# Kernel optimization log

Measured on AMD Instinct MI355X. Metric: run time of the kernel, lower is better.

The kernel has to match this reference:

```python
import jax, jax.numpy as jnp
import numpy as np

N = 50000
E = 600000
F_IN = 128
F_OUT = 128


def setup_inputs() -> dict:
    key = jax.random.key(0)
    k = jax.random.split(key, 8)
    x = jax.random.normal(k[0], (N, F_IN), dtype=jnp.float32)
    edge_index = jax.random.randint(k[1], (2, E), 0, N, dtype=jnp.int64)
    edge_weight = jax.random.uniform(k[2], (E,), dtype=jnp.float32)
    # glorot-initialized linear params (w1 is dead code in the original, kept for faithfulness)
    s = float(np.sqrt(6.0 / (F_IN + F_OUT)))
    W1 = jax.random.uniform(k[3], (F_IN, F_OUT), minval=-s, maxval=s, dtype=jnp.float32)
    b1 = jnp.zeros((F_OUT,), dtype=jnp.float32)
    W2 = jax.random.uniform(k[4], (F_IN, F_OUT), minval=-s, maxval=s, dtype=jnp.float32)
    b2 = jnp.zeros((F_OUT,), dtype=jnp.float32)
    a = jnp.full((1,), 0.5, dtype=jnp.float32)
    b = jnp.full((1,), 0.5, dtype=jnp.float32)
    return {"x": x, "edge_index": edge_index, "edge_weight": edge_weight,
            "W1": W1, "b1": b1, "W2": W2, "b2": b2, "a": a, "b": b}


def reference(x, edge_index, edge_weight, W1, b1, W2, b2, a, b):
    # wh_1 = self.w1(x)  (computed but unused in the original forward)
    wh_1 = x @ W1 + b1  # noqa: F841 (dead, DCE'd under jit)
    src, dst = edge_index[0], edge_index[1]
    # gather neighbor features [E, F_IN], scatter-sum to destination nodes [N, F_IN]
    x_j = jax.ops.segment_sum(x[src], dst, num_segments=N)
    wh_2 = x_j @ W2 + b2
    return wh_2
```

## Files before the change

kernel.cpp:

```cpp
#include <hip/hip_runtime.h>

#define F 128
#define CAP 64
#define LDT 136
#define TR 64
#define KC 32
#define LDA 36
#define LDW 160

typedef __attribute__((ext_vector_type(8))) short bf16x8;
typedef __attribute__((ext_vector_type(4))) float f32x4;

__device__ __forceinline__ unsigned short bf16r(float f)
{
    unsigned u = __float_as_uint(f);
    return (unsigned short)((u + 0x7fffu + ((u >> 16) & 1u)) >> 16);
}

__device__ __forceinline__ void load_edge(const int* __restrict__ ei, int is64,
                                          int E, int e, int& s, int& d)
{
    if (is64) {
        s = reinterpret_cast<const int2*>(ei)[e].x;
        d = reinterpret_cast<const int2*>(ei)[(size_t)E + e].x;
    } else {
        s = ei[e];
        d = ei[E + e];
    }
}

__global__ __launch_bounds__(256) void prep_kernel(
    const int* __restrict__ ei, const float* __restrict__ x,
    const float* __restrict__ W, int* __restrict__ flag,
    int* __restrict__ cursor, unsigned int* __restrict__ xh,
    unsigned short* __restrict__ Wt, int N, int M)
{
    int i = blockIdx.x * 256 + threadIdx.x;
    if (i < M) {
        float2 v = reinterpret_cast<const float2*>(x)[i];
        xh[i] = (unsigned)bf16r(v.x) | ((unsigned)bf16r(v.y) << 16);
    }
    if (i < N) cursor[i] = 0;
    if (i < F * F) {
        int k = i >> 7, n = i & 127;
        Wt[n * F + k] = bf16r(W[i]);
    }
    if (i == 0) {
        int or_hi = ei[1] | ei[3] | ei[5] | ei[7] | ei[9] | ei[11] | ei[13] | ei[15];
        *flag = (or_hi == 0) ? 1 : 0;
    }
}

__global__ __launch_bounds__(256) void position4_kernel(
    const int* __restrict__ ei, const int* __restrict__ flag_p,
    int* __restrict__ cursor, unsigned short* __restrict__ csr16, int E)
{
    const int tid = blockIdx.x * 256 + threadIdx.x;
    const int base = 4 * tid;
    if (base >= E) return;
    const int is64 = *flag_p;

    int s[4], d[4];
    int cnt;
    if (base + 3 < E && (E & 3) == 0) {
        cnt = 4;
        if (is64) {
            const int4* sp = reinterpret_cast<const int4*>(ei);
            int4 a = sp[tid * 2], b = sp[tid * 2 + 1];
            s[0] = a.x; s[1] = a.z; s[2] = b.x; s[3] = b.z;
            const int4* dp = reinterpret_cast<const int4*>(ei) + ((size_t)E >> 1);
            int4 c = dp[tid * 2], e4 = dp[tid * 2 + 1];
            d[0] = c.x; d[1] = c.z; d[2] = e4.x; d[3] = e4.z;
        } else {
            int4 sv = reinterpret_cast<const int4*>(ei)[tid];
            int4 dv = reinterpret_cast<const int4*>(ei + E)[tid];
            s[0] = sv.x; s[1] = sv.y; s[2] = sv.z; s[3] = sv.w;
            d[0] = dv.x; d[1] = dv.y; d[2] = dv.z; d[3] = dv.w;
        }
    } else {
        cnt = E - base; if (cnt > 4) cnt = 4;
        for (int j = 0; j < cnt; ++j) load_edge(ei, is64, E, base + j, s[j], d[j]);
        for (int j = cnt; j < 4; ++j) { s[j] = 0; d[j] = 0; }
    }

    int slot[4];
    #pragma unroll
    for (int j = 0; j < 4; ++j)
        slot[j] = (j < cnt) ? atomicAdd(&cursor[d[j]], 1) : CAP;
    #pragma unroll
    for (int j = 0; j < 4; ++j)
        if (slot[j] < CAP) csr16[(size_t)d[j] * CAP + slot[j]] = (unsigned short)s[j];
}

__device__ __forceinline__ float4 bf16x4_to_f4(uint2 u)
{
    float4 f;
    f.x = __uint_as_float(u.x << 16);
    f.y = __uint_as_float(u.x & 0xffff0000u);
    f.z = __uint_as_float(u.y << 16);
    f.w = __uint_as_float(u.y & 0xffff0000u);
    return f;
}

__global__ __launch_bounds__(256) void gather_bucket_kernel(
    const unsigned int* __restrict__ xh, const int* __restrict__ ei,
    const int* __restrict__ flag_p, const int* __restrict__ cursor,
    const unsigned short* __restrict__ csr16, unsigned int* __restrict__ aggbf,
    int N, int E)
{
    int node = blockIdx.x * 4 + (threadIdx.x >> 6);
    if (node >= N) return;
    int lane = threadIdx.x & 63;
    int half = lane >> 5;
    int col = lane & 31;
    int deg = cursor[node];

    const uint2* x2 = reinterpret_cast<const uint2*>(xh);
    float4 a0 = make_float4(0.f, 0.f, 0.f, 0.f);
    float4 a1 = make_float4(0.f, 0.f, 0.f, 0.f);

    if (deg <= CAP) {
        int sv = (lane < deg) ? (int)csr16[(size_t)node * CAP + lane] : 0;
        int i = 0;
        for (; i + 3 < deg; i += 4) {
            int e0 = __shfl(sv, i + half);
            int e1 = __shfl(sv, i + 2 + half);
            float4 v0 = bf16x4_to_f4(x2[(size_t)e0 * 32 + col]);
            float4 v1 = bf16x4_to_f4(x2[(size_t)e1 * 32 + col]);
            a0.x += v0.x; a0.y += v0.y; a0.z += v0.z; a0.w += v0.w;
            a1.x += v1.x; a1.y += v1.y; a1.z += v1.z; a1.w += v1.w;
        }
        for (; i + 1 < deg; i += 2) {
            int e0 = __shfl(sv, i + half);
            float4 v0 = bf16x4_to_f4(x2[(size_t)e0 * 32 + col]);
            a0.x += v0.x; a0.y += v0.y; a0.z += v0.z; a0.w += v0.w;
        }
        if (i < deg) {
            int e0 = __shfl(sv, i);
            if (half == 0) {
                float4 v = bf16x4_to_f4(x2[(size_t)e0 * 32 + col]);
                a0.x += v.x; a0.y += v.y; a0.z += v.z; a0.w += v.w;
            }
        }
    } else {
        int is64 = *flag_p;
        for (int base = 0; base < E; base += 64) {
            int e = base + lane;
            int s = 0, d = -1;
            if (e < E) load_edge(ei, is64, E, e, s, d);
            unsigned long long m = __ballot(d == node);
            while (m) {
                int i = __ffsll((long long)m) - 1;
                m &= m - 1;
                int sb = __shfl(s, i);
                float4 v = bf16x4_to_f4(x2[(size_t)sb * 32 + col]);
                if (half == 0) { a0.x += v.x; a0.y += v.y; a0.z += v.z; a0.w += v.w; }
            }
        }
    }
    a0.x += a1.x; a0.y += a1.y; a0.z += a1.z; a0.w += a1.w;
    a0.x += __shfl_xor(a0.x, 32);
    a0.y += __shfl_xor(a0.y, 32);
    a0.z += __shfl_xor(a0.z, 32);
    a0.w += __shfl_xor(a0.w, 32);
    if (half == 0) {
        uint2 o;
        o.x = (unsigned)bf16r(a0.x) | ((unsigned)bf16r(a0.y) << 16);
        o.y = (unsigned)bf16r(a0.z) | ((unsigned)bf16r(a0.w) << 16);
        reinterpret_cast<uint2*>(aggbf)[(size_t)node * 32 + col] = o;
    }
}

__global__ __launch_bounds__(256) void gemm_mfma_kernel(
    const unsigned short* __restrict__ aggbf, const unsigned short* __restrict__ Wt,
    const float* __restrict__ bias, float* __restrict__ out, int N)
{
    __shared__ unsigned short sWt[F * LDT];
    const int t = threadIdx.x;

    const uint4* Wg = reinterpret_cast<const uint4*>(Wt);
    #pragma unroll
    for (int u = 0; u < 8; ++u) {
        int idx = u * 256 + t;
        int n = idx >> 4;
        int c = idx & 15;
        *reinterpret_cast<uint4*>(&sWt[n * LDT + c * 8]) = Wg[idx];
    }
    __syncthreads();

    const int wv = t >> 6, lane = t & 63;
    const int quad = lane >> 4, n15 = lane & 15;
    const int rbase = blockIdx.x * 64 + wv * 16;

    f32x4 acc[8];
    #pragma unroll
    for (int i = 0; i < 8; ++i) acc[i] = (f32x4){0.f, 0.f, 0.f, 0.f};

    const int arow = rbase + n15;
    const bool aval = (arow < N);
    #pragma unroll
    for (int kc = 0; kc < F; kc += 32) {
        bf16x8 af;
        if (aval)
            af = *reinterpret_cast<const bf16x8*>(aggbf + (size_t)arow * F + kc + quad * 8);
        else
            af = (bf16x8){0, 0, 0, 0, 0, 0, 0, 0};
        #pragma unroll
        for (int nt = 0; nt < 8; ++nt) {
            bf16x8 bfr = *reinterpret_cast<const bf16x8*>(
                &sWt[(nt * 16 + n15) * LDT + kc + quad * 8]);
            acc[nt] = __builtin_amdgcn_mfma_f32_16x16x32_bf16(af, bfr, acc[nt], 0, 0, 0);
        }
    }

    #pragma unroll
    for (int nt = 0; nt < 8; ++nt) {
        float bv = bias[nt * 16 + n15];
        #pragma unroll
        for (int reg = 0; reg < 4; ++reg) {
            int row = rbase + quad * 4 + reg;
            if (row < N)
                out[(size_t)row * F + nt * 16 + n15] = acc[nt][reg] + bv;
        }
    }
}

__global__ __launch_bounds__(256) void init_kernel(
    const int* __restrict__ ei, int* __restrict__ flag,
    int* __restrict__ zero_arr, int N)
{
    int i = blockIdx.x * 256 + threadIdx.x;
    if (i < N) zero_arr[i] = 0;
    if (i == 0) {
        int or_hi = ei[1] | ei[3] | ei[5] | ei[7] | ei[9] | ei[11] | ei[13] | ei[15];
        *flag = (or_hi == 0) ? 1 : 0;
    }
}

__global__ __launch_bounds__(256) void position_bucket_kernel(
    const int* __restrict__ ei, const int* __restrict__ flag_p,
    int* __restrict__ cursor, int* __restrict__ csr_src, int E)
{
    int e = blockIdx.x * 256 + threadIdx.x;
    if (e >= E) return;
    int s, d;
    load_edge(ei, *flag_p, E, e, s, d);
    int slot = atomicAdd(&cursor[d], 1);
    if (slot < CAP) csr_src[(size_t)d * CAP + slot] = s;
}

__global__ __launch_bounds__(256) void gather_bucket_f32_kernel(
    const float* __restrict__ x, const int* __restrict__ ei,
    const int* __restrict__ flag_p, const int* __restrict__ cursor,
    const int* __restrict__ csr_src, float* __restrict__ agg, int N, int E)
{
    int node = blockIdx.x * 4 + (threadIdx.x >> 6);
    if (node >= N) return;
    int lane = threadIdx.x & 63;
    int half = lane >> 5;
    int col = lane & 31;
    int deg = cursor[node];

    const float4* x4 = reinterpret_cast<const float4*>(x);
    float4 a0 = make_float4(0.f, 0.f, 0.f, 0.f);
    float4 a1 = make_float4(0.f, 0.f, 0.f, 0.f);

    if (deg <= CAP) {
        int sv = (lane < deg) ? csr_src[(size_t)node * CAP + lane] : 0;
        int i = 0;
        for (; i + 3 < deg; i += 4) {
            int e0 = __shfl(sv, i + half);
            int e1 = __shfl(sv, i + 2 + half);
            float4 v0 = x4[(size_t)e0 * 32 + col];
            float4 v1 = x4[(size_t)e1 * 32 + col];
            a0.x += v0.x; a0.y += v0.y; a0.z += v0.z; a0.w += v0.w;
            a1.x += v1.x; a1.y += v1.y; a1.z += v1.z; a1.w += v1.w;
        }
        for (; i + 1 < deg; i += 2) {
            int e0 = __shfl(sv, i + half);
            float4 v0 = x4[(size_t)e0 * 32 + col];
            a0.x += v0.x; a0.y += v0.y; a0.z += v0.z; a0.w += v0.w;
        }
        if (i < deg) {
            int e0 = __shfl(sv, i);
            if (half == 0) {
                float4 v = x4[(size_t)e0 * 32 + col];
                a0.x += v.x; a0.y += v.y; a0.z += v.z; a0.w += v.w;
            }
        }
    } else {
        int is64 = *flag_p;
        for (int base = 0; base < E; base += 64) {
            int e = base + lane;
            int s = 0, d = -1;
            if (e < E) load_edge(ei, is64, E, e, s, d);
            unsigned long long m = __ballot(d == node);
            while (m) {
                int i = __ffsll((long long)m) - 1;
                m &= m - 1;
                int sb = __shfl(s, i);
                float4 v = x4[(size_t)sb * 32 + col];
                if (half == 0) { a0.x += v.x; a0.y += v.y; a0.z += v.z; a0.w += v.w; }
            }
        }
    }
    a0.x += a1.x; a0.y += a1.y; a0.z += a1.z; a0.w += a1.w;
    a0.x += __shfl_xor(a0.x, 32);
    a0.y += __shfl_xor(a0.y, 32);
    a0.z += __shfl_xor(a0.z, 32);
    a0.w += __shfl_xor(a0.w, 32);
    if (half == 0)
        reinterpret_cast<float4*>(agg)[(size_t)node * 32 + col] = a0;
}

__global__ __launch_bounds__(256) void scatter_kernel(
    const float* __restrict__ x, const int* __restrict__ ei,
    const int* __restrict__ flag_p, float* __restrict__ agg, int E)
{
    int tid = blockIdx.x * 256 + threadIdx.x;
    int e = tid >> 5;
    if (e >= E) return;
    int c = (tid & 31) << 2;
    int s, d;
    load_edge(ei, *flag_p, E, e, s, d);
    float4 v = *reinterpret_cast<const float4*>(x + (size_t)s * F + c);
    float* o = agg + (size_t)d * F + c;
    unsafeAtomicAdd(o + 0, v.x);
    unsafeAtomicAdd(o + 1, v.y);
    unsafeAtomicAdd(o + 2, v.z);
    unsafeAtomicAdd(o + 3, v.w);
}

__global__ __launch_bounds__(256) void gemm_kernel(
    float* __restrict__ io, const float* __restrict__ W,
    const float* __restrict__ bias, int N)
{
    __shared__ float sA[TR * LDA];
    __shared__ float sW[KC * LDW];
    const int t = threadIdx.x;
    const int row0 = blockIdx.x * TR;
    const int g = t & 7;
    const int r = t >> 3;

    float acc[2][16];
    #pragma unroll
    for (int i = 0; i < 2; ++i)
        #pragma unroll
        for (int j = 0; j < 16; ++j) acc[i][j] = 0.0f;

    for (int kc = 0; kc < F; kc += KC) {
        #pragma unroll
        for (int u = 0; u < 2; ++u) {
            int idx = u * 256 + t;
            int row = idx >> 3;
            int k4 = (idx & 7) * 4;
            int grow = row0 + row;
            float4 v = (grow < N)
                ? *reinterpret_cast<const float4*>(io + (size_t)grow * F + kc + k4)
                : make_float4(0.f, 0.f, 0.f, 0.f);
            *reinterpret_cast<float4*>(&sA[row * LDA + k4]) = v;
        }
        #pragma unroll
        for (int u = 0; u < 4; ++u) {
            int idx = u * 256 + t;
            int kk = idx >> 5;
            int f4 = (idx & 31) * 4;
            float4 v = *reinterpret_cast<const float4*>(W + (size_t)(kc + kk) * F + f4);
            int chunk = f4 >> 4;
            int within = f4 & 15;
            *reinterpret_cast<float4*>(&sW[kk * LDW + chunk * 20 + within]) = v;
        }
        __syncthreads();

        #pragma unroll 8
        for (int kk = 0; kk < KC; ++kk) {
            const float* wp = &sW[kk * LDW + g * 20];
            const float4 w0 = *reinterpret_cast<const float4*>(wp + 0);
            const float4 w1 = *reinterpret_cast<const float4*>(wp + 4);
            const float4 w2 = *reinterpret_cast<const float4*>(wp + 8);
            const float4 w3 = *reinterpret_cast<const float4*>(wp + 12);
            #pragma unroll
            for (int i = 0; i < 2; ++i) {
                const float xv = sA[(r * 2 + i) * LDA + kk];
                acc[i][0]  += xv * w0.x;  acc[i][1]  += xv * w0.y;
                acc[i][2]  += xv * w0.z;  acc[i][3]  += xv * w0.w;
                acc[i][4]  += xv * w1.x;  acc[i][5]  += xv * w1.y;
                acc[i][6]  += xv * w1.z;  acc[i][7]  += xv * w1.w;
                acc[i][8]  += xv * w2.x;  acc[i][9]  += xv * w2.y;
                acc[i][10] += xv * w2.z;  acc[i][11] += xv * w2.w;
                acc[i][12] += xv * w3.x;  acc[i][13] += xv * w3.y;
                acc[i][14] += xv * w3.z;  acc[i][15] += xv * w3.w;
            }
        }
        __syncthreads();
    }

    float bv[16];
    #pragma unroll
    for (int j = 0; j < 16; ++j) bv[j] = bias[g * 16 + j];
    #pragma unroll
    for (int i = 0; i < 2; ++i) {
        int row = row0 + r * 2 + i;
        if (row < N) {
            float* o = io + (size_t)row * F + g * 16;
            #pragma unroll
            for (int j4 = 0; j4 < 4; ++j4) {
                float4 v;
                v.x = acc[i][j4 * 4 + 0] + bv[j4 * 4 + 0];
                v.y = acc[i][j4 * 4 + 1] + bv[j4 * 4 + 1];
                v.z = acc[i][j4 * 4 + 2] + bv[j4 * 4 + 2];
                v.w = acc[i][j4 * 4 + 3] + bv[j4 * 4 + 3];
                *reinterpret_cast<float4*>(o + j4 * 4) = v;
            }
        }
    }
}

extern "C" void kernel_launch(void* const* d_in, const int* in_sizes, int n_in,
                              void* d_out, int out_size, void* d_ws, size_t ws_size,
                              hipStream_t stream) {
    const float* x  = (const float*)d_in[0];
    const int*   ei = (const int*)d_in[1];
    const float* W2 = (const float*)d_in[5];
    const float* b2 = (const float*)d_in[6];
    float* out = (float*)d_out;

    const int N = in_sizes[0] / F;
    const int E = in_sizes[2];
    const int nblk = (N + 255) / 256;
    const int M = N * (F / 2);
    const int eblk = (E + 255) / 256;

    int* ws = (int*)d_ws;
    size_t needA = (size_t)16 * 4 + (size_t)N * 4 + (size_t)N * CAP * 2
                 + (size_t)M * 4 + (size_t)F * F * 2 + (size_t)N * (F / 2) * 4;
    size_t needB = (size_t)(16 + N + (size_t)N * CAP) * sizeof(int);

    if (ws_size >= needA && N <= 65536) {
        int* flag    = ws;
        int* cursor  = flag + 16;
        unsigned short* csr16 = (unsigned short*)(cursor + N);
        unsigned int*   xh    = (unsigned int*)(csr16 + (size_t)N * CAP);
        unsigned short* Wt    = (unsigned short*)(xh + M);
        unsigned int*   aggbf = (unsigned int*)(Wt + F * F);

        int pmax = M; if (N > pmax) pmax = N; if (F * F > pmax) pmax = F * F;
        prep_kernel<<<(pmax + 255) / 256, 256, 0, stream>>>(
            ei, x, W2, flag, cursor, xh, Wt, N, M);
        int pblk = ((E + 3) / 4 + 255) / 256;
        position4_kernel<<<pblk, 256, 0, stream>>>(ei, flag, cursor, csr16, E);
        gather_bucket_kernel<<<(N + 3) / 4, 256, 0, stream>>>(
            xh, ei, flag, cursor, csr16, aggbf, N, E);
        gemm_mfma_kernel<<<(N + 63) / 64, 256, 0, stream>>>(
            (const unsigned short*)aggbf, Wt, b2, out, N);
    } else if (ws_size >= needB) {
        int* flag    = ws;
        int* cursor  = flag + 16;
        int* csr_src = cursor + N;
        init_kernel<<<nblk, 256, 0, stream>>>(ei, flag, cursor, N);
        position_bucket_kernel<<<eblk, 256, 0, stream>>>(ei, flag, cursor, csr_src, E);
        gather_bucket_f32_kernel<<<(N + 3) / 4, 256, 0, stream>>>(
            x, ei, flag, cursor, csr_src, out, N, E);
        gemm_kernel<<<(N + TR - 1) / TR, 256, 0, stream>>>(out, W2, b2, N);
    } else {
        int* flag = ws;
        init_kernel<<<1, 64, 0, stream>>>(ei, flag, flag + 16, 0);
        hipMemsetAsync(out, 0, (size_t)N * F * sizeof(float), stream);
        scatter_kernel<<<(E * 32 + 255) / 256, 256, 0, stream>>>(x, ei, flag, out, E);
        gemm_kernel<<<(N + TR - 1) / TR, 256, 0, stream>>>(out, W2, b2, N);
    }
}
```

Before: 161.5 us.

## Fuse gather into MFMA GEMM via shared memory and merge prep with CSR build

Each GEMM block now builds its 64 aggregated rows itself: every wave walks 16 nodes with a prefetched next-node CSR list and writes bf16 sums into LDS, so the aggbf round trip through global memory and one launch go away. The x/W conversion and the edge bucketing are merged into one kernel, which computes the int64 flag inline, and the cursor array is zeroed with a memset. The price is less parallelism in the gather (one wave serially handles 16 nodes, about 782 blocks), a larger LDS footprint that may limit occupancy, and a new race: the bf16 copy of x is written in the same kernel that fills the CSR, but it is only read by the next kernel, so that part is safe.

```diff
diff --git a/kernel.cpp b/kernel.cpp
--- a/kernel.cpp
+++ b/kernel.cpp
@@ -17,6 +17,11 @@
     return (unsigned short)((u + 0x7fffu + ((u >> 16) & 1u)) >> 16);
 }
 
+__device__ __forceinline__ unsigned pack2(float a, float b)
+{
+    return (unsigned)bf16r(a) | ((unsigned)bf16r(b) << 16);
+}
+
 __device__ __forceinline__ void load_edge(const int* __restrict__ ei, int is64,
                                           int E, int e, int& s, int& d)
 {
@@ -29,36 +34,40 @@
     }
 }
 
-__global__ __launch_bounds__(256) void prep_kernel(
+__device__ __forceinline__ float4 bf16x4_to_f4(uint2 u)
+{
+    float4 f;
+    f.x = __uint_as_float(u.x << 16);
+    f.y = __uint_as_float(u.x & 0xffff0000u);
+    f.z = __uint_as_float(u.y << 16);
+    f.w = __uint_as_float(u.y & 0xffff0000u);
+    return f;
+}
+
+__global__ __launch_bounds__(256) void prep_pos_kernel(
     const int* __restrict__ ei, const float* __restrict__ x,
-    const float* __restrict__ W, int* __restrict__ flag,
-    int* __restrict__ cursor, unsigned int* __restrict__ xh,
-    unsigned short* __restrict__ Wt, int N, int M)
-{
-    int i = blockIdx.x * 256 + threadIdx.x;
-    if (i < M) {
-        float2 v = reinterpret_cast<const float2*>(x)[i];
-        xh[i] = (unsigned)bf16r(v.x) | ((unsigned)bf16r(v.y) << 16);
-    }
-    if (i < N) cursor[i] = 0;
-    if (i < F * F) {
-        int k = i >> 7, n = i & 127;
-        Wt[n * F + k] = bf16r(W[i]);
-    }
-    if (i == 0) {
-        int or_hi = ei[1] | ei[3] | ei[5] | ei[7] | ei[9] | ei[11] | ei[13] | ei[15];
-        *flag = (or_hi == 0) ? 1 : 0;
-    }
-}
-
-__global__ __launch_bounds__(256) void position4_kernel(
-    const int* __restrict__ ei, const int* __restrict__ flag_p,
-    int* __restrict__ cursor, unsigned short* __restrict__ csr16, int E)
+    const float* __restrict__ W, int* __restrict__ cursor,
+    unsigned short* __restrict__ csr16, unsigned int* __restrict__ xh,
+    unsigned short* __restrict__ Wt, int N, int E, int M4)
 {
     const int tid = blockIdx.x * 256 + threadIdx.x;
+
+    if (tid < M4) {
+        float4 v = reinterpret_cast<const float4*>(x)[tid];
+        uint2 o;
+        o.x = pack2(v.x, v.y);
+        o.y = pack2(v.z, v.w);
+        reinterpret_cast<uint2*>(xh)[tid] = o;
+    }
+    if (tid < F * F) {
+        int k = tid >> 7, n = tid & 127;
+        Wt[n * F + k] = bf16r(W[tid]);
+    }
+
     const int base = 4 * tid;
     if (base >= E) return;
-    const int is64 = *flag_p;
+    int or_hi = ei[1] | ei[3] | ei[5] | ei[7] | ei[9] | ei[11] | ei[13] | ei[15];
+    const int is64 = (or_hi == 0) ? 1 : 0;
 
     int s[4], d[4];
     int cnt;
@@ -92,90 +101,14 @@
         if (slot[j] < CAP) csr16[(size_t)d[j] * CAP + slot[j]] = (unsigned short)s[j];
 }
 
-__device__ __forceinline__ float4 bf16x4_to_f4(uint2 u)
-{
-    float4 f;
-    f.x = __uint_as_float(u.x << 16);
-    f.y = __uint_as_float(u.x & 0xffff0000u);
-    f.z = __uint_as_float(u.y << 16);
-    f.w = __uint_as_float(u.y & 0xffff0000u);
-    return f;
-}
-
-__global__ __launch_bounds__(256) void gather_bucket_kernel(
+__global__ __launch_bounds__(256) void gather_gemm_kernel(
     const unsigned int* __restrict__ xh, const int* __restrict__ ei,
-    const int* __restrict__ flag_p, const int* __restrict__ cursor,
-    const unsigned short* __restrict__ csr16, unsigned int* __restrict__ aggbf,
-    int N, int E)
-{
-    int node = blockIdx.x * 4 + (threadIdx.x >> 6);
-    if (node >= N) return;
-    int lane = threadIdx.x & 63;
-    int half = lane >> 5;
-    int col = lane & 31;
-    int deg = cursor[node];
-
-    const uint2* x2 = reinterpret_cast<const uint2*>(xh);
-    float4 a0 = make_float4(0.f, 0.f, 0.f, 0.f);
-    float4 a1 = make_float4(0.f, 0.f, 0.f, 0.f);
-
-    if (deg <= CAP) {
-        int sv = (lane < deg) ? (int)csr16[(size_t)node * CAP + lane] : 0;
-        int i = 0;
-        for (; i + 3 < deg; i += 4) {
-            int e0 = __shfl(sv, i + half);
-            int e1 = __shfl(sv, i + 2 + half);
-            float4 v0 = bf16x4_to_f4(x2[(size_t)e0 * 32 + col]);
-            float4 v1 = bf16x4_to_f4(x2[(size_t)e1 * 32 + col]);
-            a0.x += v0.x; a0.y += v0.y; a0.z += v0.z; a0.w += v0.w;
-            a1.x += v1.x; a1.y += v1.y; a1.z += v1.z; a1.w += v1.w;
-        }
-        for (; i + 1 < deg; i += 2) {
-            int e0 = __shfl(sv, i + half);
-            float4 v0 = bf16x4_to_f4(x2[(size_t)e0 * 32 + col]);
-            a0.x += v0.x; a0.y += v0.y; a0.z += v0.z; a0.w += v0.w;
-        }
-        if (i < deg) {
-            int e0 = __shfl(sv, i);
-            if (half == 0) {
-                float4 v = bf16x4_to_f4(x2[(size_t)e0 * 32 + col]);
-                a0.x += v.x; a0.y += v.y; a0.z += v.z; a0.w += v.w;
-            }
-        }
-    } else {
-        int is64 = *flag_p;
-        for (int base = 0; base < E; base += 64) {
-            int e = base + lane;
-            int s = 0, d = -1;
-            if (e < E) load_edge(ei, is64, E, e, s, d);
-            unsigned long long m = __ballot(d == node);
-            while (m) {
-                int i = __ffsll((long long)m) - 1;
-                m &= m - 1;
-                int sb = __shfl(s, i);
-                float4 v = bf16x4_to_f4(x2[(size_t)sb * 32 + col]);
-                if (half == 0) { a0.x += v.x; a0.y += v.y; a0.z += v.z; a0.w += v.w; }
-            }
-        }
-    }
-    a0.x += a1.x; a0.y += a1.y; a0.z += a1.z; a0.w += a1.w;
-    a0.x += __shfl_xor(a0.x, 32);
-    a0.y += __shfl_xor(a0.y, 32);
-    a0.z += __shfl_xor(a0.z, 32);
-    a0.w += __shfl_xor(a0.w, 32);
-    if (half == 0) {
-        uint2 o;
-        o.x = (unsigned)bf16r(a0.x) | ((unsigned)bf16r(a0.y) << 16);
-        o.y = (unsigned)bf16r(a0.z) | ((unsigned)bf16r(a0.w) << 16);
-        reinterpret_cast<uint2*>(aggbf)[(size_t)node * 32 + col] = o;
-    }
-}
-
-__global__ __launch_bounds__(256) void gemm_mfma_kernel(
-    const unsigned short* __restrict__ aggbf, const unsigned short* __restrict__ Wt,
-    const float* __restrict__ bias, float* __restrict__ out, int N)
+    const int* __restrict__ cursor, const unsigned short* __restrict__ csr16,
+    const unsigned short* __restrict__ Wt, const float* __restrict__ bias,
+    float* __restrict__ out, int N, int E)
 {
     __shared__ unsigned short sWt[F * LDT];
+    __shared__ unsigned short sA[64 * LDT];
     const int t = threadIdx.x;
 
     const uint4* Wg = reinterpret_cast<const uint4*>(Wt);
@@ -186,25 +119,113 @@
         int c = idx & 15;
         *reinterpret_cast<uint4*>(&sWt[n * LDT + c * 8]) = Wg[idx];
     }
+
+    const int wv = t >> 6, lane = t & 63;
+    const int half = lane >> 5, col = lane & 31;
+    const int nbase = blockIdx.x * 64 + wv * 16;
+    const uint2* x2 = reinterpret_cast<const uint2*>(xh);
+
+    int degl = 0;
+    {
+        int myn = nbase + (lane & 15);
+        if (lane < 16 && myn < N) degl = cursor[myn];
+    }
+
+    int node = nbase;
+    int deg = __shfl(degl, 0);
+    int sv = 0;
+    if (node < N && deg <= CAP && lane < deg)
+        sv = (int)csr16[(size_t)node * CAP + lane];
+
+    for (int ni = 0; ni < 16; ++ni) {
+        int nnode = node + 1;
+        int ndeg = (ni < 15) ? __shfl(degl, ni + 1) : 0;
+        int nsv = 0;
+        if (ni < 15 && nnode < N && ndeg <= CAP && lane < ndeg)
+            nsv = (int)csr16[(size_t)nnode * CAP + lane];
+
+        float4 a0 = make_float4(0.f, 0.f, 0.f, 0.f);
+        float4 a1 = make_float4(0.f, 0.f, 0.f, 0.f);
+        if (node < N) {
+            if (deg <= CAP) {
+                int i = 0;
+                for (; i + 7 < deg; i += 8) {
+                    int e0 = __shfl(sv, i + half);
+                    int e1 = __shfl(sv, i + 2 + half);
+                    int e2 = __shfl(sv, i + 4 + half);
+                    int e3 = __shfl(sv, i + 6 + half);
+                    float4 v0 = bf16x4_to_f4(x2[(size_t)e0 * 32 + col]);
+                    float4 v1 = bf16x4_to_f4(x2[(size_t)e1 * 32 + col]);
+                    float4 v2 = bf16x4_to_f4(x2[(size_t)e2 * 32 + col]);
+                    float4 v3 = bf16x4_to_f4(x2[(size_t)e3 * 32 + col]);
+                    a0.x += v0.x; a0.y += v0.y; a0.z += v0.z; a0.w += v0.w;
+                    a1.x += v1.x; a1.y += v1.y; a1.z += v1.z; a1.w += v1.w;
+                    a0.x += v2.x; a0.y += v2.y; a0.z += v2.z; a0.w += v2.w;
+                    a1.x += v3.x; a1.y += v3.y; a1.z += v3.z; a1.w += v3.w;
+                }
+                for (; i + 3 < deg; i += 4) {
+                    int e0 = __shfl(sv, i + half);
+                    int e1 = __shfl(sv, i + 2 + half);
+                    float4 v0 = bf16x4_to_f4(x2[(size_t)e0 * 32 + col]);
+                    float4 v1 = bf16x4_to_f4(x2[(size_t)e1 * 32 + col]);
+                    a0.x += v0.x; a0.y += v0.y; a0.z += v0.z; a0.w += v0.w;
+                    a1.x += v1.x; a1.y += v1.y; a1.z += v1.z; a1.w += v1.w;
+                }
+                for (; i + 1 < deg; i += 2) {
+                    int e0 = __shfl(sv, i + half);
+                    float4 v0 = bf16x4_to_f4(x2[(size_t)e0 * 32 + col]);
+                    a0.x += v0.x; a0.y += v0.y; a0.z += v0.z; a0.w += v0.w;
+                }
+                if (i < deg) {
+                    int e0 = __shfl(sv, i);
+                    if (half == 0) {
+                        float4 v = bf16x4_to_f4(x2[(size_t)e0 * 32 + col]);
+                        a0.x += v.x; a0.y += v.y; a0.z += v.z; a0.w += v.w;
+                    }
+                }
+            } else {
+                int or_hi = ei[1] | ei[3] | ei[5] | ei[7] | ei[9] | ei[11] | ei[13] | ei[15];
+                int is64 = (or_hi == 0) ? 1 : 0;
+                for (int base = 0; base < E; base += 64) {
+                    int e = base + lane;
+                    int ss = 0, dd = -1;
+                    if (e < E) load_edge(ei, is64, E, e, ss, dd);
+                    unsigned long long m = __ballot(dd == node);
+                    while (m) {
+                        int i = __ffsll((long long)m) - 1;
+                        m &= m - 1;
+                        int sb = __shfl(ss, i);
+                        float4 v = bf16x4_to_f4(x2[(size_t)sb * 32 + col]);
+                        if (half == 0) { a0.x += v.x; a0.y += v.y; a0.z += v.z; a0.w += v.w; }
+                    }
+                }
+            }
+        }
+        a0.x += a1.x; a0.y += a1.y; a0.z += a1.z; a0.w += a1.w;
+        a0.x += __shfl_xor(a0.x, 32);
+        a0.y += __shfl_xor(a0.y, 32);
+        a0.z += __shfl_xor(a0.z, 32);
+        a0.w += __shfl_xor(a0.w, 32);
+        if (half == 0) {
+            uint2 o;
+            o.x = pack2(a0.x, a0.y);
+            o.y = pack2(a0.z, a0.w);
+            *reinterpret_cast<uint2*>(&sA[(wv * 16 + ni) * LDT + col * 4]) = o;
+        }
+        node = nnode; deg = ndeg; sv = nsv;
+    }
+
     __syncthreads();
 
-    const int wv = t >> 6, lane = t & 63;
     const int quad = lane >> 4, n15 = lane & 15;
-    const int rbase = blockIdx.x * 64 + wv * 16;
-
     f32x4 acc[8];
     #pragma unroll
     for (int i = 0; i < 8; ++i) acc[i] = (f32x4){0.f, 0.f, 0.f, 0.f};
 
-    const int arow = rbase + n15;
-    const bool aval = (arow < N);
     #pragma unroll
     for (int kc = 0; kc < F; kc += 32) {
-        bf16x8 af;
-        if (aval)
-            af = *reinterpret_cast<const bf16x8*>(aggbf + (size_t)arow * F + kc + quad * 8);
-        else
-            af = (bf16x8){0, 0, 0, 0, 0, 0, 0, 0};
+        bf16x8 af = *reinterpret_cast<const bf16x8*>(
+            &sA[(wv * 16 + n15) * LDT + kc + quad * 8]);
         #pragma unroll
         for (int nt = 0; nt < 8; ++nt) {
             bf16x8 bfr = *reinterpret_cast<const bf16x8*>(
@@ -213,6 +234,7 @@
         }
     }
 
+    const int rbase = blockIdx.x * 64 + wv * 16;
     #pragma unroll
     for (int nt = 0; nt < 8; ++nt) {
         float bv = bias[nt * 16 + n15];
@@ -416,6 +438,8 @@
     }
 }
 
+static inline size_t al16(size_t v) { return (v + 15) & ~(size_t)15; }
+
 extern "C" void kernel_launch(void* const* d_in, const int* in_sizes, int n_in,
                               void* d_out, int out_size, void* d_ws, size_t ws_size,
                               hipStream_t stream) {
@@ -428,42 +452,45 @@
     const int N = in_sizes[0] / F;
     const int E = in_sizes[2];
     const int nblk = (N + 255) / 256;
-    const int M = N * (F / 2);
     const int eblk = (E + 255) / 256;
 
-    int* ws = (int*)d_ws;
-    size_t needA = (size_t)16 * 4 + (size_t)N * 4 + (size_t)N * CAP * 2
-                 + (size_t)M * 4 + (size_t)F * F * 2 + (size_t)N * (F / 2) * 4;
+    char* wsb = (char*)d_ws;
+    size_t off = 64;
+    int* cursor = (int*)(wsb + off);
+    off = al16(off + (size_t)N * 4);
+    unsigned short* csr16 = (unsigned short*)(wsb + off);
+    off = al16(off + (size_t)N * CAP * 2);
+    unsigned int* xh = (unsigned int*)(wsb + off);
+    off = al16(off + (size_t)N * (F / 2) * 4);
+    unsigned short* Wt = (unsigned short*)(wsb + off);
+    off += (size_t)F * F * 2;
+    size_t needA = off;
+
     size_t needB = (size_t)(16 + N + (size_t)N * CAP) * sizeof(int);
 
     if (ws_size >= needA && N <= 65536) {
-        int* flag    = ws;
-        int* cursor  = flag + 16;
-        unsigned short* csr16 = (unsigned short*)(cursor + N);
-        unsigned int*   xh    = (unsigned int*)(csr16 + (size_t)N * CAP);
-        unsigned short* Wt    = (unsigned short*)(xh + M);
-        unsigned int*   aggbf = (unsigned int*)(Wt + F * F);
-
-        int pmax = M; if (N > pmax) pmax = N; if (F * F > pmax) pmax = F * F;
-        prep_kernel<<<(pmax + 255) / 256, 256, 0, stream>>>(
-            ei, x, W2, flag, cursor, xh, Wt, N, M);
-        int pblk = ((E + 3) / 4 + 255) / 256;
-        position4_kernel<<<pblk, 256, 0, stream>>>(ei, flag, cursor, csr16, E);
-        gather_bucket_kernel<<<(N + 3) / 4, 256, 0, stream>>>(
-            xh, ei, flag, cursor, csr16, aggbf, N, E);
-        gemm_mfma_kernel<<<(N + 63) / 64, 256, 0, stream>>>(
-            (const unsigned short*)aggbf, Wt, b2, out, N);
+        hipMemsetAsync(cursor, 0, (size_t)N * sizeof(int), stream);
+
+        const int M4 = N * (F / 4);
+        int gp = (M4 + 255) / 256;
+        int ge = (((E + 3) / 4) + 255) / 256; if (ge > gp) gp = ge;
+        int gw = (F * F + 255) / 256;         if (gw > gp) gp = gw;
+        prep_pos_kernel<<<gp, 256, 0, stream>>>(
+            ei, x, W2, cursor, csr16, xh, Wt, N, E, M4);
+
+        gather_gemm_kernel<<<(N + 63) / 64, 256, 0, stream>>>(
+            xh, ei, cursor, csr16, Wt, b2, out, N, E);
     } else if (ws_size >= needB) {
-        int* flag    = ws;
-        int* cursor  = flag + 16;
-        int* csr_src = cursor + N;
-        init_kernel<<<nblk, 256, 0, stream>>>(ei, flag, cursor, N);
-        position_bucket_kernel<<<eblk, 256, 0, stream>>>(ei, flag, cursor, csr_src, E);
+        int* flag    = (int*)wsb;
+        int* curs    = flag + 16;
+        int* csr_src = curs + N;
+        init_kernel<<<nblk, 256, 0, stream>>>(ei, flag, curs, N);
+        position_bucket_kernel<<<eblk, 256, 0, stream>>>(ei, flag, curs, csr_src, E);
         gather_bucket_f32_kernel<<<(N + 3) / 4, 256, 0, stream>>>(
-            x, ei, flag, cursor, csr_src, out, N, E);
+            x, ei, flag, curs, csr_src, out, N, E);
         gemm_kernel<<<(N + TR - 1) / TR, 256, 0, stream>>>(out, W2, b2, N);
     } else {
-        int* flag = ws;
+        int* flag = (int*)wsb;
         init_kernel<<<1, 64, 0, stream>>>(ei, flag, flag + 16, 0);
         hipMemsetAsync(out, 0, (size_t)N * F * sizeof(float), stream);
         scatter_kernel<<<(E * 32 + 255) / 256, 256, 0, stream>>>(x, ei, flag, out, E);
```

Measured after the change: 194.4 us. 1.2x slower.

## Gather neighbor rows via async global-to-LDS copies and widen prep conversion

Applied to the files above, without the earlier changes.

Replaces the register-based neighbor gather with global_load_lds async 16-byte copies that stage up to 16 neighbor rows per wave in LDS, then accumulate 8 bf16 values per lane with a cross-lane reduction. The aim is more bytes per load instruction and more loads in flight, hiding gather latency. The prep kernel also converts x to bf16 four floats per thread instead of two. The change adds LDS use, explicit waitcnt barriers that serialize each chunk, and wasted lanes when degree is not a multiple of 4.

```diff
diff --git a/kernel.cpp b/kernel.cpp
--- a/kernel.cpp
+++ b/kernel.cpp
@@ -17,6 +17,11 @@
     return (unsigned short)((u + 0x7fffu + ((u >> 16) & 1u)) >> 16);
 }
 
+__device__ __forceinline__ unsigned pack2(float a, float b)
+{
+    return (unsigned)bf16r(a) | ((unsigned)bf16r(b) << 16);
+}
+
 __device__ __forceinline__ void load_edge(const int* __restrict__ ei, int is64,
                                           int E, int e, int& s, int& d)
 {
@@ -29,16 +34,37 @@
     }
 }
 
+__device__ __forceinline__ float4 bf16x4_to_f4(uint2 u)
+{
+    float4 f;
+    f.x = __uint_as_float(u.x << 16);
+    f.y = __uint_as_float(u.x & 0xffff0000u);
+    f.z = __uint_as_float(u.y << 16);
+    f.w = __uint_as_float(u.y & 0xffff0000u);
+    return f;
+}
+
+__device__ __forceinline__ void async_copy16(const void* g, void* lds)
+{
+    __builtin_amdgcn_global_load_lds(
+        (const __attribute__((address_space(1))) unsigned int*)g,
+        (__attribute__((address_space(3))) unsigned int*)lds,
+        16, 0, 0);
+}
+
 __global__ __launch_bounds__(256) void prep_kernel(
     const int* __restrict__ ei, const float* __restrict__ x,
     const float* __restrict__ W, int* __restrict__ flag,
     int* __restrict__ cursor, unsigned int* __restrict__ xh,
-    unsigned short* __restrict__ Wt, int N, int M)
+    unsigned short* __restrict__ Wt, int N, int M4)
 {
     int i = blockIdx.x * 256 + threadIdx.x;
-    if (i < M) {
-        float2 v = reinterpret_cast<const float2*>(x)[i];
-        xh[i] = (unsigned)bf16r(v.x) | ((unsigned)bf16r(v.y) << 16);
+    if (i < M4) {
+        float4 v = reinterpret_cast<const float4*>(x)[i];
+        uint2 o;
+        o.x = pack2(v.x, v.y);
+        o.y = pack2(v.z, v.w);
+        reinterpret_cast<uint2*>(xh)[i] = o;
     }
     if (i < N) cursor[i] = 0;
     if (i < F * F) {
@@ -92,58 +118,77 @@
         if (slot[j] < CAP) csr16[(size_t)d[j] * CAP + slot[j]] = (unsigned short)s[j];
 }
 
-__device__ __forceinline__ float4 bf16x4_to_f4(uint2 u)
-{
-    float4 f;
-    f.x = __uint_as_float(u.x << 16);
-    f.y = __uint_as_float(u.x & 0xffff0000u);
-    f.z = __uint_as_float(u.y << 16);
-    f.w = __uint_as_float(u.y & 0xffff0000u);
-    return f;
-}
-
-__global__ __launch_bounds__(256) void gather_bucket_kernel(
+__global__ __launch_bounds__(256, 8) void gather_async_kernel(
     const unsigned int* __restrict__ xh, const int* __restrict__ ei,
     const int* __restrict__ flag_p, const int* __restrict__ cursor,
     const unsigned short* __restrict__ csr16, unsigned int* __restrict__ aggbf,
     int N, int E)
 {
-    int node = blockIdx.x * 4 + (threadIdx.x >> 6);
+    __shared__ char stg[4][4096];
+    const int node = blockIdx.x * 4 + (threadIdx.x >> 6);
     if (node >= N) return;
-    int lane = threadIdx.x & 63;
-    int half = lane >> 5;
-    int col = lane & 31;
-    int deg = cursor[node];
-
-    const uint2* x2 = reinterpret_cast<const uint2*>(xh);
-    float4 a0 = make_float4(0.f, 0.f, 0.f, 0.f);
-    float4 a1 = make_float4(0.f, 0.f, 0.f, 0.f);
+    const int wv   = threadIdx.x >> 6;
+    const int lane = threadIdx.x & 63;
+    const int eg   = lane >> 4;
+    const int c    = lane & 15;
+    char* ldsW = &stg[wv][0];
+
+    const int deg = cursor[node];
 
     if (deg <= CAP) {
         int sv = (lane < deg) ? (int)csr16[(size_t)node * CAP + lane] : 0;
-        int i = 0;
-        for (; i + 3 < deg; i += 4) {
-            int e0 = __shfl(sv, i + half);
-            int e1 = __shfl(sv, i + 2 + half);
-            float4 v0 = bf16x4_to_f4(x2[(size_t)e0 * 32 + col]);
-            float4 v1 = bf16x4_to_f4(x2[(size_t)e1 * 32 + col]);
-            a0.x += v0.x; a0.y += v0.y; a0.z += v0.z; a0.w += v0.w;
-            a1.x += v1.x; a1.y += v1.y; a1.z += v1.z; a1.w += v1.w;
-        }
-        for (; i + 1 < deg; i += 2) {
-            int e0 = __shfl(sv, i + half);
-            float4 v0 = bf16x4_to_f4(x2[(size_t)e0 * 32 + col]);
-            a0.x += v0.x; a0.y += v0.y; a0.z += v0.z; a0.w += v0.w;
-        }
-        if (i < deg) {
-            int e0 = __shfl(sv, i);
-            if (half == 0) {
-                float4 v = bf16x4_to_f4(x2[(size_t)e0 * 32 + col]);
-                a0.x += v.x; a0.y += v.y; a0.z += v.z; a0.w += v.w;
-            }
+        float f[8];
+        #pragma unroll
+        for (int j = 0; j < 8; ++j) f[j] = 0.f;
+
+        for (int ch = 0; ch < deg; ch += 16) {
+            int nE = deg - ch; if (nE > 16) nE = 16;
+            int nL = (nE + 3) >> 2;
+            if (ch > 0) {
+                asm volatile("s_waitcnt lgkmcnt(0)" ::: "memory");
+                __builtin_amdgcn_sched_barrier(0);
+            }
+            for (int l = 0; l < nL; ++l) {
+                int e = ch + l * 4 + eg;
+                int esel = (e < deg) ? e : (deg - 1);
+                int src = __shfl(sv, esel);
+                async_copy16((const char*)xh + ((size_t)src * 256 + (size_t)c * 16),
+                             ldsW + l * 1024);
+            }
+            asm volatile("s_waitcnt vmcnt(0)" ::: "memory");
+            __builtin_amdgcn_sched_barrier(0);
+            for (int l = 0; l < nL; ++l) {
+                uint4 v = *reinterpret_cast<const uint4*>(ldsW + l * 1024 + lane * 16);
+                if (ch + l * 4 + eg < deg) {
+                    f[0] += __uint_as_float(v.x << 16);
+                    f[1] += __uint_as_float(v.x & 0xffff0000u);
+                    f[2] += __uint_as_float(v.y << 16);
+                    f[3] += __uint_as_float(v.y & 0xffff0000u);
+                    f[4] += __uint_as_float(v.z << 16);
+                    f[5] += __uint_as_float(v.z & 0xffff0000u);
+                    f[6] += __uint_as_float(v.w << 16);
+                    f[7] += __uint_as_float(v.w & 0xffff0000u);
+                }
+            }
+        }
+        #pragma unroll
+        for (int j = 0; j < 8; ++j) {
+            f[j] += __shfl_xor(f[j], 16);
+            f[j] += __shfl_xor(f[j], 32);
+        }
+        if (eg == 0) {
+            uint4 o;
+            o.x = pack2(f[0], f[1]);
+            o.y = pack2(f[2], f[3]);
+            o.z = pack2(f[4], f[5]);
+            o.w = pack2(f[6], f[7]);
+            reinterpret_cast<uint4*>(aggbf)[(size_t)node * 16 + c] = o;
         }
     } else {
+        const int half = lane >> 5, col = lane & 31;
+        const uint2* x2 = reinterpret_cast<const uint2*>(xh);
         int is64 = *flag_p;
+        float4 a0 = make_float4(0.f, 0.f, 0.f, 0.f);
         for (int base = 0; base < E; base += 64) {
             int e = base + lane;
             int s = 0, d = -1;
@@ -157,17 +202,16 @@
                 if (half == 0) { a0.x += v.x; a0.y += v.y; a0.z += v.z; a0.w += v.w; }
             }
         }
-    }
-    a0.x += a1.x; a0.y += a1.y; a0.z += a1.z; a0.w += a1.w;
-    a0.x += __shfl_xor(a0.x, 32);
-    a0.y += __shfl_xor(a0.y, 32);
-    a0.z += __shfl_xor(a0.z, 32);
-    a0.w += __shfl_xor(a0.w, 32);
-    if (half == 0) {
-        uint2 o;
-        o.x = (unsigned)bf16r(a0.x) | ((unsigned)bf16r(a0.y) << 16);
-        o.y = (unsigned)bf16r(a0.z) | ((unsigned)bf16r(a0.w) << 16);
-        reinterpret_cast<uint2*>(aggbf)[(size_t)node * 32 + col] = o;
+        a0.x += __shfl_xor(a0.x, 32);
+        a0.y += __shfl_xor(a0.y, 32);
+        a0.z += __shfl_xor(a0.z, 32);
+        a0.w += __shfl_xor(a0.w, 32);
+        if (half == 0) {
+            uint2 o;
+            o.x = pack2(a0.x, a0.y);
+            o.y = pack2(a0.z, a0.w);
+            reinterpret_cast<uint2*>(aggbf)[(size_t)node * 32 + col] = o;
+        }
     }
 }
 
@@ -429,6 +473,7 @@
     const int E = in_sizes[2];
     const int nblk = (N + 255) / 256;
     const int M = N * (F / 2);
+    const int M4 = N * (F / 4);
     const int eblk = (E + 255) / 256;
 
     int* ws = (int*)d_ws;
@@ -444,12 +489,12 @@
         unsigned short* Wt    = (unsigned short*)(xh + M);
         unsigned int*   aggbf = (unsigned int*)(Wt + F * F);
 
-        int pmax = M; if (N > pmax) pmax = N; if (F * F > pmax) pmax = F * F;
+        int pmax = M4; if (N > pmax) pmax = N; if (F * F > pmax) pmax = F * F;
         prep_kernel<<<(pmax + 255) / 256, 256, 0, stream>>>(
-            ei, x, W2, flag, cursor, xh, Wt, N, M);
+            ei, x, W2, flag, cursor, xh, Wt, N, M4);
         int pblk = ((E + 3) / 4 + 255) / 256;
         position4_kernel<<<pblk, 256, 0, stream>>>(ei, flag, cursor, csr16, E);
-        gather_bucket_kernel<<<(N + 3) / 4, 256, 0, stream>>>(
+        gather_async_kernel<<<(N + 3) / 4, 256, 0, stream>>>(
             xh, ei, flag, cursor, csr16, aggbf, N, E);
         gemm_mfma_kernel<<<(N + 63) / 64, 256, 0, stream>>>(
             (const unsigned short*)aggbf, Wt, b2, out, N);
```

Result: no change. 158.4 us (-1.9%).
